# Optimization experiments

Hardware: AMD Instinct MI355X
Metric: run time of the kernel (lower is better)

The kernel has to match this reference:

```python
import jax, jax.numpy as jnp
import numpy as np

B, S, D = 2, 2048, 1024
H = 16
HD = D // H


def setup_inputs() -> dict:
    key = jax.random.key(0)
    ks = jax.random.split(key, 6)
    x = jax.random.normal(ks[0], (B, S, D), dtype=jnp.float32)
    scale = 1.0 / np.sqrt(D)
    Wq = jax.random.normal(ks[1], (D, D), dtype=jnp.float32) * scale
    Wk = jax.random.normal(ks[2], (D, D), dtype=jnp.float32) * scale
    Wv = jax.random.normal(ks[3], (D, D), dtype=jnp.float32) * scale
    Wo = jax.random.normal(ks[4], (D, D), dtype=jnp.float32) * scale
    bo = jax.random.normal(ks[5], (D,), dtype=jnp.float32) * 0.01
    return {"x": x, "Wq": Wq, "Wk": Wk, "Wv": Wv, "Wo": Wo, "bo": bo}


def reference(x, Wq, Wk, Wv, Wo, bo):
    b, t, _ = x.shape
    # QKV projections (no bias), split into heads: [b, h, t, hd]
    q = (x @ Wq).reshape(b, t, H, HD).transpose(0, 2, 1, 3)
    k = (x @ Wk).reshape(b, t, H, HD).transpose(0, 2, 1, 3)
    v = (x @ Wv).reshape(b, t, H, HD).transpose(0, 2, 1, 3)
    # scores [b, h, t, t]; causal mask (upper triangle -> -inf) applied before scaling
    scores = jnp.einsum("bhqd,bhkd->bhqk", q, k)
    causal = jnp.triu(jnp.ones((t, t), dtype=bool), k=1)
    scores = jnp.where(causal, -jnp.inf, scores)
    attn = jax.nn.softmax(scores / jnp.sqrt(jnp.asarray(HD, scores.dtype)), axis=-1)
    ctx = jnp.einsum("bhqk,bhkd->bhqd", attn, v)
    ctx = ctx.transpose(0, 2, 1, 3).reshape(b, t, H * HD)
    return ctx @ Wo + bo
```

## Files before the change

kernel.cpp:

```cpp
#include <hip/hip_runtime.h>

#define B_ 2
#define S_ 2048
#define D_ 1024
#define H_ 16
#define HD_ 64
#define M_ (B_*S_)

typedef __attribute__((ext_vector_type(8))) short bf16x8;
typedef __attribute__((ext_vector_type(4))) short s16x4;
typedef __attribute__((ext_vector_type(4))) float f32x4;
typedef __attribute__((ext_vector_type(4))) unsigned int u32x4;

static __device__ __forceinline__ unsigned short f2bf(float f) {
  unsigned int u = __builtin_bit_cast(unsigned int, f);
  u += 0x7FFFu + ((u >> 16) & 1u);
  return (unsigned short)(u >> 16);
}

static __device__ __forceinline__ unsigned int cvt_pk_bf16(float a, float b) {
  unsigned int r;
  asm("v_cvt_pk_bf16_f32 %0, %1, %2" : "=v"(r) : "v"(a), "v"(b));
  return r;
}

static __device__ __forceinline__ void gload_lds16(const void* g, void* l) {
  __builtin_amdgcn_global_load_lds(
      (const __attribute__((address_space(1))) unsigned int*)g,
      (__attribute__((address_space(3))) unsigned int*)l, 16, 0, 0);
}

__global__ __launch_bounds__(256) void xcvt_kernel(const float* __restrict__ x,
                                                   unsigned short* __restrict__ xb) {
  size_t i = ((size_t)blockIdx.x * 256 + threadIdx.x) * 8;
  float4 a = ((const float4*)(x + i))[0];
  float4 b = ((const float4*)(x + i))[1];
  bf16x8 w;
  w[0]=(short)f2bf(a.x); w[1]=(short)f2bf(a.y); w[2]=(short)f2bf(a.z); w[3]=(short)f2bf(a.w);
  w[4]=(short)f2bf(b.x); w[5]=(short)f2bf(b.y); w[6]=(short)f2bf(b.z); w[7]=(short)f2bf(b.w);
  *(bf16x8*)(xb + i) = w;
}

__global__ void wtrans_kernel(const float* __restrict__ Wq, const float* __restrict__ Wk,
                              const float* __restrict__ Wv, const float* __restrict__ Wo,
                              unsigned short* __restrict__ wt) {
  __shared__ float tile[32][33];
  const float* W = blockIdx.z==0 ? Wq : blockIdx.z==1 ? Wk : blockIdx.z==2 ? Wv : Wo;
  unsigned short* out = wt + (size_t)blockIdx.z * D_ * D_;
  int n0 = blockIdx.x*32, k0 = blockIdx.y*32;
  int tx = threadIdx.x, ty = threadIdx.y;
  #pragma unroll
  for (int i=0;i<4;i++) tile[ty+i*8][tx] = W[(size_t)(k0+ty+i*8)*D_ + n0+tx];
  __syncthreads();
  #pragma unroll
  for (int i=0;i<4;i++) out[(size_t)(n0+ty+i*8)*D_ + (k0+tx)] = f2bf(tile[tx][ty+i*8]);
}

#define GEMM_K_LOOP(Abase, Bbase)                                                     \
  for (int ks = 0; ks < 16; ++ks) {                                                   \
    const int k0 = ks * 64;                                                           \
    __syncthreads();                                                                  \
    _Pragma("unroll")                                                                 \
    for (int p = 0; p < 4; ++p) {                                                     \
      int c = p*256 + t;                                                              \
      int row = c >> 3, sl = (c & 7) ^ (row & 7);                                     \
      gload_lds16(Abase + (size_t)row*D_ + k0 + sl*8, &As[(p*256 + wid*64)*8]);       \
    }                                                                                 \
    _Pragma("unroll")                                                                 \
    for (int p = 0; p < 4; ++p) {                                                     \
      int c = p*256 + t;                                                              \
      int row = c >> 3, sl = (c & 7) ^ (row & 7);                                     \
      gload_lds16(Bbase + (size_t)row*D_ + k0 + sl*8, &Bs[(p*256 + wid*64)*8]);       \
    }                                                                                 \
    __syncthreads();                                                                  \
    _Pragma("unroll")                                                                 \
    for (int kk = 0; kk < 2; ++kk) {                                                  \
      bf16x8 af[4], bfr[4];                                                           \
      _Pragma("unroll")                                                               \
      for (int m = 0; m < 4; ++m) {                                                   \
        int row = wr + m*16 + l15;                                                    \
        af[m] = *(const bf16x8*)((const char*)As + row*128 + (((kk*4+lg)^(row&7))<<4)); \
      }                                                                               \
      _Pragma("unroll")                                                               \
      for (int n = 0; n < 4; ++n) {                                                   \
        int row = wc + n*16 + l15;                                                    \
        bfr[n] = *(const bf16x8*)((const char*)Bs + row*128 + (((kk*4+lg)^(row&7))<<4)); \
      }                                                                               \
      _Pragma("unroll")                                                               \
      for (int m = 0; m < 4; ++m)                                                     \
        _Pragma("unroll")                                                             \
        for (int n = 0; n < 4; ++n)                                                   \
          acc[m][n] = __builtin_amdgcn_mfma_f32_16x16x32_bf16(af[m], bfr[n], acc[m][n], 0,0,0); \
    }                                                                                 \
  }

__global__ __launch_bounds__(256,3) void gemm_qkv_kernel(
    const unsigned short* __restrict__ xb, const unsigned short* __restrict__ wt,
    unsigned short* __restrict__ Qo, unsigned short* __restrict__ Ko,
    unsigned short* __restrict__ Vto) {
  __shared__ __align__(16) unsigned short As[128*64];
  __shared__ __align__(16) unsigned short Bs[128*64];
  const int z = blockIdx.z;
  const int m0 = blockIdx.y*128, n0 = blockIdx.x*128;
  const int t = threadIdx.x, lane = t & 63, wid = t >> 6;
  const int wr = (wid>>1)*64, wc = (wid&1)*64;
  const int l15 = lane & 15, lg = lane >> 4;
  const unsigned short* Ab = xb + (size_t)m0 * D_;
  const unsigned short* Bb = wt + (size_t)z * D_ * D_ + (size_t)n0 * D_;

  f32x4 acc[4][4];
  #pragma unroll
  for (int m=0;m<4;m++)
    #pragma unroll
    for (int n=0;n<4;n++) acc[m][n] = f32x4{0.f,0.f,0.f,0.f};

  GEMM_K_LOOP(Ab, Bb)

  const float qscale = 0.18033688011112042f;
  #pragma unroll
  for (int m=0;m<4;m++) {
    #pragma unroll
    for (int n=0;n<4;n++) {
      #pragma unroll
      for (int r=0;r<4;r++) {
        int gm = m0 + wr + m*16 + lg*4 + r;
        int gn = n0 + wc + n*16 + l15;
        int b = gm >> 11, s = gm & (S_-1);
        int h = gn >> 6,  d = gn & 63;
        float av = acc[m][n][r];
        if (z==0) av *= qscale;
        unsigned short val = f2bf(av);
        if (z==0)      Qo[(((size_t)(b*H_+h))*S_ + s)*HD_ + d] = val;
        else if (z==1) Ko[(((size_t)(b*H_+h))*S_ + s)*HD_ + d] = val;
        else           Vto[(((size_t)(b*H_+h))*HD_ + d)*S_ + s] = val;
      }
    }
  }
}

__global__ __launch_bounds__(256,4) void attn_kernel(
    const unsigned short* __restrict__ Q, const unsigned short* __restrict__ K,
    const unsigned short* __restrict__ Vt, unsigned short* __restrict__ ctx) {
  __shared__ __align__(16) unsigned short KT[2][64*64];
  __shared__ __align__(16) unsigned short VT[2][64*64];
  const int t = threadIdx.x, lane = t & 63, wid = t >> 6;
  const int bh = blockIdx.x & 31;
  const int qt = 31 - (int)(blockIdx.x >> 5);
  const int b = bh >> 4, h = bh & 15;
  const int q0 = qt * 64, qw0 = q0 + wid * 16;
  const int nchunk = qt + 1;
  const unsigned short* Qp = Q  + (size_t)bh * S_ * HD_;
  const unsigned short* Kp = K  + (size_t)bh * S_ * HD_;
  const unsigned short* Vp = Vt + (size_t)bh * HD_ * S_;
  const int l15 = lane & 15, lg = lane >> 4;
  const int rsub = lane >> 3, slot = lane & 7;
  const int sslot = slot ^ rsub;

  bf16x8 qf0 = *(const bf16x8*)(Qp + (size_t)(qw0 + l15)*HD_ + lg*8);
  bf16x8 qf1 = *(const bf16x8*)(Qp + (size_t)(qw0 + l15)*HD_ + 32 + lg*8);

  f32x4 o[4];
  #pragma unroll
  for (int dt=0;dt<4;dt++) o[dt] = f32x4{0.f,0.f,0.f,0.f};
  float lsum = 0.f;

  auto stage = [&](int ch, int buf) {
    const int kk0 = ch * 64;
    #pragma unroll
    for (int j=0;j<2;j++) {
      int row = 16*wid + 8*j + rsub;
      gload_lds16(Kp + (size_t)(kk0 + row)*HD_ + sslot*8, &KT[buf][(16*wid + 8*j)*64]);
      gload_lds16(Vp + (size_t)row*S_ + kk0 + sslot*8,    &VT[buf][(16*wid + 8*j)*64]);
    }
  };

  stage(0, 0);
  __syncthreads();

  for (int ch=0; ch<nchunk; ++ch) {
    const int cur = ch & 1;
    const int kk0 = ch * 64;
    if (ch + 1 < nchunk) stage(ch+1, cur^1);

    const char* Kt = (const char*)&KT[cur][0];
    const char* Vv = (const char*)&VT[cur][0];

    f32x4 st[4];
    __builtin_amdgcn_s_setprio(1);
    #pragma unroll
    for (int kt=0; kt<4; ++kt) {
      int row = kt*16 + l15;
      int sw = (row & 7) << 4;
      bf16x8 kf0 = *(const bf16x8*)(Kt + row*128 + ((lg*16)      ^ sw));
      bf16x8 kf1 = *(const bf16x8*)(Kt + row*128 + ((64 + lg*16) ^ sw));
      f32x4 z = f32x4{0.f,0.f,0.f,0.f};
      z = __builtin_amdgcn_mfma_f32_16x16x32_bf16(kf0, qf0, z, 0,0,0);
      z = __builtin_amdgcn_mfma_f32_16x16x32_bf16(kf1, qf1, z, 0,0,0);
      st[kt] = z;
    }
    __builtin_amdgcn_s_setprio(0);

    if (ch == nchunk-1) {
      const int q = qw0 + l15;
      #pragma unroll
      for (int kt=0;kt<4;kt++)
        #pragma unroll
        for (int r=0;r<4;r++)
          if (kk0 + kt*16 + lg*4 + r > q) st[kt][r] = -INFINITY;
    }

    s16x4 pa[4];
    #pragma unroll
    for (int kt=0;kt<4;kt++) {
      #pragma unroll
      for (int r=0;r<4;r++) {
        float p = exp2f(st[kt][r]);
        st[kt][r] = p;
        lsum += p;
      }
      unsigned int plo = cvt_pk_bf16(st[kt][0], st[kt][1]);
      unsigned int phi = cvt_pk_bf16(st[kt][2], st[kt][3]);
      uint2 u; u.x = plo; u.y = phi;
      pa[kt] = __builtin_bit_cast(s16x4, u);
    }

    __builtin_amdgcn_s_setprio(1);
    #pragma unroll
    for (int dt=0;dt<4;dt++) {
      int row = dt*16 + l15;
      int sw = (row & 7) << 4;
      const char* vrow = Vv + row*128;
      #pragma unroll
      for (int kt=0;kt<4;kt++) {
        s16x4 vb = *(const s16x4*)(vrow + ((kt*32 + lg*8) ^ sw));
        o[dt] = __builtin_amdgcn_mfma_f32_16x16x16bf16_1k(pa[kt], vb, o[dt], 0,0,0);
      }
    }
    __builtin_amdgcn_s_setprio(0);

    __syncthreads();
  }

  lsum += __shfl_xor(lsum, 16);
  lsum += __shfl_xor(lsum, 32);
  float li = 1.f / lsum;
  float lr[4];
  #pragma unroll
  for (int r=0;r<4;r++) lr[r] = __shfl(li, lg*4 + r);
  #pragma unroll
  for (int dt=0;dt<4;dt++)
    #pragma unroll
    for (int r=0;r<4;r++) {
      size_t row = (size_t)(b*S_ + qw0 + lg*4 + r);
      ctx[row*D_ + h*HD_ + dt*16 + l15] = f2bf(o[dt][r] * lr[r]);
    }
}

__global__ __launch_bounds__(256,3) void gemm_out_kernel(
    const unsigned short* __restrict__ ctx, const unsigned short* __restrict__ WtO,
    const float* __restrict__ bo, float* __restrict__ out) {
  __shared__ __align__(16) unsigned short As[128*64];
  __shared__ __align__(16) unsigned short Bs[128*64];
  const int m0 = blockIdx.y*128, n0 = blockIdx.x*128;
  const int t = threadIdx.x, lane = t & 63, wid = t >> 6;
  const int wr = (wid>>1)*64, wc = (wid&1)*64;
  const int l15 = lane & 15, lg = lane >> 4;
  const unsigned short* Ab = ctx + (size_t)m0 * D_;
  const unsigned short* Bb = WtO + (size_t)n0 * D_;

  f32x4 acc[4][4];
  #pragma unroll
  for (int m=0;m<4;m++)
    #pragma unroll
    for (int n=0;n<4;n++) acc[m][n] = f32x4{0.f,0.f,0.f,0.f};

  GEMM_K_LOOP(Ab, Bb)

  #pragma unroll
  for (int n=0;n<4;n++) {
    float bias = bo[n0 + wc + n*16 + l15];
    #pragma unroll
    for (int m=0;m<4;m++)
      #pragma unroll
      for (int r=0;r<4;r++) {
        int gm = m0 + wr + m*16 + lg*4 + r;
        int gn = n0 + wc + n*16 + l15;
        out[(size_t)gm*D_ + gn] = acc[m][n][r] + bias;
      }
  }
}

extern "C" void kernel_launch(void* const* d_in, const int* in_sizes, int n_in,
                              void* d_out, int out_size, void* d_ws, size_t ws_size,
                              hipStream_t stream) {
  (void)in_sizes; (void)n_in; (void)out_size; (void)ws_size;
  const float* x  = (const float*)d_in[0];
  const float* Wq = (const float*)d_in[1];
  const float* Wk = (const float*)d_in[2];
  const float* Wv = (const float*)d_in[3];
  const float* Wo = (const float*)d_in[4];
  const float* bo = (const float*)d_in[5];
  float* out = (float*)d_out;

  unsigned short* wt  = (unsigned short*)d_ws;
  unsigned short* Qb  = wt  + (size_t)4*D_*D_;
  unsigned short* Kb  = Qb  + (size_t)M_*D_;
  unsigned short* Vtb = Kb  + (size_t)M_*D_;
  unsigned short* ctb = Vtb + (size_t)M_*D_;
  unsigned short* xbb = ctb + (size_t)M_*D_;

  xcvt_kernel<<<dim3(M_*D_/(256*8)), 256, 0, stream>>>(x, xbb);
  wtrans_kernel<<<dim3(32,32,4), dim3(32,8), 0, stream>>>(Wq, Wk, Wv, Wo, wt);
  gemm_qkv_kernel<<<dim3(8,32,3), 256, 0, stream>>>(xbb, wt, Qb, Kb, Vtb);
  attn_kernel<<<dim3(1024), 256, 0, stream>>>(Qb, Kb, Vtb, ctb);
  gemm_out_kernel<<<dim3(8,32), 256, 0, stream>>>(ctb, wt + (size_t)3*D_*D_, bo, out);
}
```

Measured before the change: 113.5 us.

## Pair causal query tiles per block to balance work and share K/V loads

Each attention block now handles two query tiles, pr and 31-pr, so every block performs the same total of 33 key chunks, and the grid is halved to 512 blocks. The K/V tiles staged in LDS are reused by both query tiles for the chunks they share, which cuts global/LDS traffic for those chunks. The cost is more registers per thread (two sets of accumulators and Q fragments), which may lower occupancy under the 256x4 launch bound, and fewer blocks to spread across the CUs.

```diff
diff --git a/kernel.cpp b/kernel.cpp
--- a/kernel.cpp
+++ b/kernel.cpp
@@ -1,4 +1,5 @@
 #include <hip/hip_runtime.h>
+#include <type_traits>
 
 #define B_ 2
 #define S_ 2048
@@ -145,10 +146,11 @@
   __shared__ __align__(16) unsigned short VT[2][64*64];
   const int t = threadIdx.x, lane = t & 63, wid = t >> 6;
   const int bh = blockIdx.x & 31;
-  const int qt = 31 - (int)(blockIdx.x >> 5);
+  const int pr = (int)(blockIdx.x >> 5);
   const int b = bh >> 4, h = bh & 15;
-  const int q0 = qt * 64, qw0 = q0 + wid * 16;
-  const int nchunk = qt + 1;
+  const int qA0 = pr*64 + wid*16;
+  const int qB0 = (31-pr)*64 + wid*16;
+  const int nA = pr + 1, nB = 32 - pr;
   const unsigned short* Qp = Q  + (size_t)bh * S_ * HD_;
   const unsigned short* Kp = K  + (size_t)bh * S_ * HD_;
   const unsigned short* Vp = Vt + (size_t)bh * HD_ * S_;
@@ -156,13 +158,15 @@
   const int rsub = lane >> 3, slot = lane & 7;
   const int sslot = slot ^ rsub;
 
-  bf16x8 qf0 = *(const bf16x8*)(Qp + (size_t)(qw0 + l15)*HD_ + lg*8);
-  bf16x8 qf1 = *(const bf16x8*)(Qp + (size_t)(qw0 + l15)*HD_ + 32 + lg*8);
-
-  f32x4 o[4];
-  #pragma unroll
-  for (int dt=0;dt<4;dt++) o[dt] = f32x4{0.f,0.f,0.f,0.f};
-  float lsum = 0.f;
+  bf16x8 qfA0 = *(const bf16x8*)(Qp + (size_t)(qA0 + l15)*HD_ + lg*8);
+  bf16x8 qfA1 = *(const bf16x8*)(Qp + (size_t)(qA0 + l15)*HD_ + 32 + lg*8);
+  bf16x8 qfB0 = *(const bf16x8*)(Qp + (size_t)(qB0 + l15)*HD_ + lg*8);
+  bf16x8 qfB1 = *(const bf16x8*)(Qp + (size_t)(qB0 + l15)*HD_ + 32 + lg*8);
+
+  f32x4 oA[4], oB[4];
+  #pragma unroll
+  for (int dt=0;dt<4;dt++) { oA[dt]=f32x4{0.f,0.f,0.f,0.f}; oB[dt]=f32x4{0.f,0.f,0.f,0.f}; }
+  float lsA = 0.f, lsB = 0.f;
 
   auto stage = [&](int ch, int buf) {
     const int kk0 = ch * 64;
@@ -174,18 +178,13 @@
     }
   };
 
-  stage(0, 0);
-  __syncthreads();
-
-  for (int ch=0; ch<nchunk; ++ch) {
-    const int cur = ch & 1;
+  auto chunk_body = [&](int ch, int cur, auto doA_c) {
+    constexpr bool DOA = decltype(doA_c)::value;
     const int kk0 = ch * 64;
-    if (ch + 1 < nchunk) stage(ch+1, cur^1);
-
     const char* Kt = (const char*)&KT[cur][0];
     const char* Vv = (const char*)&VT[cur][0];
 
-    f32x4 st[4];
+    f32x4 stA[4], stB[4];
     __builtin_amdgcn_s_setprio(1);
     #pragma unroll
     for (int kt=0; kt<4; ++kt) {
@@ -193,35 +192,52 @@
       int sw = (row & 7) << 4;
       bf16x8 kf0 = *(const bf16x8*)(Kt + row*128 + ((lg*16)      ^ sw));
       bf16x8 kf1 = *(const bf16x8*)(Kt + row*128 + ((64 + lg*16) ^ sw));
-      f32x4 z = f32x4{0.f,0.f,0.f,0.f};
-      z = __builtin_amdgcn_mfma_f32_16x16x32_bf16(kf0, qf0, z, 0,0,0);
-      z = __builtin_amdgcn_mfma_f32_16x16x32_bf16(kf1, qf1, z, 0,0,0);
-      st[kt] = z;
+      f32x4 zB = f32x4{0.f,0.f,0.f,0.f};
+      zB = __builtin_amdgcn_mfma_f32_16x16x32_bf16(kf0, qfB0, zB, 0,0,0);
+      zB = __builtin_amdgcn_mfma_f32_16x16x32_bf16(kf1, qfB1, zB, 0,0,0);
+      stB[kt] = zB;
+      if (DOA) {
+        f32x4 zA = f32x4{0.f,0.f,0.f,0.f};
+        zA = __builtin_amdgcn_mfma_f32_16x16x32_bf16(kf0, qfA0, zA, 0,0,0);
+        zA = __builtin_amdgcn_mfma_f32_16x16x32_bf16(kf1, qfA1, zA, 0,0,0);
+        stA[kt] = zA;
+      }
     }
     __builtin_amdgcn_s_setprio(0);
 
-    if (ch == nchunk-1) {
-      const int q = qw0 + l15;
+    if (ch == nB-1) {
+      const int q = qB0 + l15;
       #pragma unroll
       for (int kt=0;kt<4;kt++)
         #pragma unroll
         for (int r=0;r<4;r++)
-          if (kk0 + kt*16 + lg*4 + r > q) st[kt][r] = -INFINITY;
-    }
-
-    s16x4 pa[4];
+          if (kk0 + kt*16 + lg*4 + r > q) stB[kt][r] = -INFINITY;
+    }
+    if (DOA && ch == nA-1) {
+      const int q = qA0 + l15;
+      #pragma unroll
+      for (int kt=0;kt<4;kt++)
+        #pragma unroll
+        for (int r=0;r<4;r++)
+          if (kk0 + kt*16 + lg*4 + r > q) stA[kt][r] = -INFINITY;
+    }
+
+    s16x4 paA[4], paB[4];
     #pragma unroll
     for (int kt=0;kt<4;kt++) {
       #pragma unroll
       for (int r=0;r<4;r++) {
-        float p = exp2f(st[kt][r]);
-        st[kt][r] = p;
-        lsum += p;
-      }
-      unsigned int plo = cvt_pk_bf16(st[kt][0], st[kt][1]);
-      unsigned int phi = cvt_pk_bf16(st[kt][2], st[kt][3]);
-      uint2 u; u.x = plo; u.y = phi;
-      pa[kt] = __builtin_bit_cast(s16x4, u);
+        float p = exp2f(stB[kt][r]); stB[kt][r] = p; lsB += p;
+        if (DOA) { float pa = exp2f(stA[kt][r]); stA[kt][r] = pa; lsA += pa; }
+      }
+      uint2 uB; uB.x = cvt_pk_bf16(stB[kt][0], stB[kt][1]);
+      uB.y = cvt_pk_bf16(stB[kt][2], stB[kt][3]);
+      paB[kt] = __builtin_bit_cast(s16x4, uB);
+      if (DOA) {
+        uint2 uA; uA.x = cvt_pk_bf16(stA[kt][0], stA[kt][1]);
+        uA.y = cvt_pk_bf16(stA[kt][2], stA[kt][3]);
+        paA[kt] = __builtin_bit_cast(s16x4, uA);
+      }
     }
 
     __builtin_amdgcn_s_setprio(1);
@@ -233,27 +249,39 @@
       #pragma unroll
       for (int kt=0;kt<4;kt++) {
         s16x4 vb = *(const s16x4*)(vrow + ((kt*32 + lg*8) ^ sw));
-        o[dt] = __builtin_amdgcn_mfma_f32_16x16x16bf16_1k(pa[kt], vb, o[dt], 0,0,0);
+        oB[dt] = __builtin_amdgcn_mfma_f32_16x16x16bf16_1k(paB[kt], vb, oB[dt], 0,0,0);
+        if (DOA) oA[dt] = __builtin_amdgcn_mfma_f32_16x16x16bf16_1k(paA[kt], vb, oA[dt], 0,0,0);
       }
     }
     __builtin_amdgcn_s_setprio(0);
-
+  };
+
+  stage(0, 0);
+  __syncthreads();
+
+  for (int ch=0; ch<nB; ++ch) {
+    const int cur = ch & 1;
+    if (ch + 1 < nB) stage(ch+1, cur^1);
+    if (ch < nA) chunk_body(ch, cur, std::true_type{});
+    else         chunk_body(ch, cur, std::false_type{});
     __syncthreads();
   }
 
-  lsum += __shfl_xor(lsum, 16);
-  lsum += __shfl_xor(lsum, 32);
-  float li = 1.f / lsum;
-  float lr[4];
-  #pragma unroll
-  for (int r=0;r<4;r++) lr[r] = __shfl(li, lg*4 + r);
-  #pragma unroll
-  for (int dt=0;dt<4;dt++)
-    #pragma unroll
-    for (int r=0;r<4;r++) {
-      size_t row = (size_t)(b*S_ + qw0 + lg*4 + r);
-      ctx[row*D_ + h*HD_ + dt*16 + l15] = f2bf(o[dt][r] * lr[r]);
-    }
+  lsA += __shfl_xor(lsA, 16); lsA += __shfl_xor(lsA, 32);
+  lsB += __shfl_xor(lsB, 16); lsB += __shfl_xor(lsB, 32);
+  float liA = 1.f / lsA, liB = 1.f / lsB;
+  #pragma unroll
+  for (int r=0;r<4;r++) {
+    float lrA = __shfl(liA, lg*4 + r);
+    float lrB = __shfl(liB, lg*4 + r);
+    size_t rowA = (size_t)(b*S_ + qA0 + lg*4 + r);
+    size_t rowB = (size_t)(b*S_ + qB0 + lg*4 + r);
+    #pragma unroll
+    for (int dt=0;dt<4;dt++) {
+      ctx[rowA*D_ + h*HD_ + dt*16 + l15] = f2bf(oA[dt][r] * lrA);
+      ctx[rowB*D_ + h*HD_ + dt*16 + l15] = f2bf(oB[dt][r] * lrB);
+    }
+  }
 }
 
 __global__ __launch_bounds__(256,3) void gemm_out_kernel(
@@ -312,6 +340,6 @@
   xcvt_kernel<<<dim3(M_*D_/(256*8)), 256, 0, stream>>>(x, xbb);
   wtrans_kernel<<<dim3(32,32,4), dim3(32,8), 0, stream>>>(Wq, Wk, Wv, Wo, wt);
   gemm_qkv_kernel<<<dim3(8,32,3), 256, 0, stream>>>(xbb, wt, Qb, Kb, Vtb);
-  attn_kernel<<<dim3(1024), 256, 0, stream>>>(Qb, Kb, Vtb, ctb);
+  attn_kernel<<<dim3(512), 256, 0, stream>>>(Qb, Kb, Vtb, ctb);
   gemm_out_kernel<<<dim3(8,32), 256, 0, stream>>>(ctb, wt + (size_t)3*D_*D_, bo, out);
 }
```

New measurement: 133.8 us. 17.9% more time.

## Load K and V fragments directly from global memory in attention kernel

Applied to the files above, without the earlier changes.

Removes the double-buffered LDS staging of K and V tiles and the per-chunk block barrier; each wave now loads its MFMA operand fragments for K and V straight from global memory into registers. This eliminates shared-memory traffic and __syncthreads, freeing LDS for occupancy. In exchange, all four waves redundantly fetch the same K/V data from global/L2 with no prefetch overlap, and the V reads are narrower 8-byte strided accesses.

```diff
diff --git a/kernel.cpp b/kernel.cpp
--- a/kernel.cpp
+++ b/kernel.cpp
@@ -141,20 +141,16 @@
 __global__ __launch_bounds__(256,4) void attn_kernel(
     const unsigned short* __restrict__ Q, const unsigned short* __restrict__ K,
     const unsigned short* __restrict__ Vt, unsigned short* __restrict__ ctx) {
-  __shared__ __align__(16) unsigned short KT[2][64*64];
-  __shared__ __align__(16) unsigned short VT[2][64*64];
   const int t = threadIdx.x, lane = t & 63, wid = t >> 6;
   const int bh = blockIdx.x & 31;
   const int qt = 31 - (int)(blockIdx.x >> 5);
   const int b = bh >> 4, h = bh & 15;
-  const int q0 = qt * 64, qw0 = q0 + wid * 16;
+  const int qw0 = qt*64 + wid*16;
   const int nchunk = qt + 1;
   const unsigned short* Qp = Q  + (size_t)bh * S_ * HD_;
   const unsigned short* Kp = K  + (size_t)bh * S_ * HD_;
   const unsigned short* Vp = Vt + (size_t)bh * HD_ * S_;
   const int l15 = lane & 15, lg = lane >> 4;
-  const int rsub = lane >> 3, slot = lane & 7;
-  const int sslot = slot ^ rsub;
 
   bf16x8 qf0 = *(const bf16x8*)(Qp + (size_t)(qw0 + l15)*HD_ + lg*8);
   bf16x8 qf1 = *(const bf16x8*)(Qp + (size_t)(qw0 + l15)*HD_ + 32 + lg*8);
@@ -164,41 +160,36 @@
   for (int dt=0;dt<4;dt++) o[dt] = f32x4{0.f,0.f,0.f,0.f};
   float lsum = 0.f;
 
-  auto stage = [&](int ch, int buf) {
+  for (int ch=0; ch<nchunk; ++ch) {
     const int kk0 = ch * 64;
-    #pragma unroll
-    for (int j=0;j<2;j++) {
-      int row = 16*wid + 8*j + rsub;
-      gload_lds16(Kp + (size_t)(kk0 + row)*HD_ + sslot*8, &KT[buf][(16*wid + 8*j)*64]);
-      gload_lds16(Vp + (size_t)row*S_ + kk0 + sslot*8,    &VT[buf][(16*wid + 8*j)*64]);
-    }
-  };
-
-  stage(0, 0);
-  __syncthreads();
-
-  for (int ch=0; ch<nchunk; ++ch) {
-    const int cur = ch & 1;
-    const int kk0 = ch * 64;
-    if (ch + 1 < nchunk) stage(ch+1, cur^1);
-
-    const char* Kt = (const char*)&KT[cur][0];
-    const char* Vv = (const char*)&VT[cur][0];
+    const unsigned short* Kc = Kp + (size_t)kk0 * HD_;
+
+    bf16x8 kf0[4], kf1[4];
+    #pragma unroll
+    for (int kt=0;kt<4;kt++) {
+      kf0[kt] = *(const bf16x8*)(Kc + (size_t)(kt*16 + l15)*HD_ + lg*8);
+      kf1[kt] = *(const bf16x8*)(Kc + (size_t)(kt*16 + l15)*HD_ + 32 + lg*8);
+    }
 
     f32x4 st[4];
     __builtin_amdgcn_s_setprio(1);
     #pragma unroll
-    for (int kt=0; kt<4; ++kt) {
-      int row = kt*16 + l15;
-      int sw = (row & 7) << 4;
-      bf16x8 kf0 = *(const bf16x8*)(Kt + row*128 + ((lg*16)      ^ sw));
-      bf16x8 kf1 = *(const bf16x8*)(Kt + row*128 + ((64 + lg*16) ^ sw));
+    for (int kt=0;kt<4;kt++) {
       f32x4 z = f32x4{0.f,0.f,0.f,0.f};
-      z = __builtin_amdgcn_mfma_f32_16x16x32_bf16(kf0, qf0, z, 0,0,0);
-      z = __builtin_amdgcn_mfma_f32_16x16x32_bf16(kf1, qf1, z, 0,0,0);
+      z = __builtin_amdgcn_mfma_f32_16x16x32_bf16(kf0[kt], qf0, z, 0,0,0);
+      z = __builtin_amdgcn_mfma_f32_16x16x32_bf16(kf1[kt], qf1, z, 0,0,0);
       st[kt] = z;
     }
     __builtin_amdgcn_s_setprio(0);
+
+    s16x4 vb[4][4];
+    #pragma unroll
+    for (int dt=0;dt<4;dt++) {
+      const unsigned short* vrow = Vp + (size_t)(dt*16 + l15)*S_ + kk0;
+      #pragma unroll
+      for (int kt=0;kt<4;kt++)
+        vb[dt][kt] = *(const s16x4*)(vrow + kt*16 + lg*4);
+    }
 
     if (ch == nchunk-1) {
       const int q = qw0 + l15;
@@ -218,27 +209,19 @@
         st[kt][r] = p;
         lsum += p;
       }
-      unsigned int plo = cvt_pk_bf16(st[kt][0], st[kt][1]);
-      unsigned int phi = cvt_pk_bf16(st[kt][2], st[kt][3]);
-      uint2 u; u.x = plo; u.y = phi;
+      uint2 u;
+      u.x = cvt_pk_bf16(st[kt][0], st[kt][1]);
+      u.y = cvt_pk_bf16(st[kt][2], st[kt][3]);
       pa[kt] = __builtin_bit_cast(s16x4, u);
     }
 
     __builtin_amdgcn_s_setprio(1);
     #pragma unroll
-    for (int dt=0;dt<4;dt++) {
-      int row = dt*16 + l15;
-      int sw = (row & 7) << 4;
-      const char* vrow = Vv + row*128;
-      #pragma unroll
-      for (int kt=0;kt<4;kt++) {
-        s16x4 vb = *(const s16x4*)(vrow + ((kt*32 + lg*8) ^ sw));
-        o[dt] = __builtin_amdgcn_mfma_f32_16x16x16bf16_1k(pa[kt], vb, o[dt], 0,0,0);
-      }
-    }
+    for (int dt=0;dt<4;dt++)
+      #pragma unroll
+      for (int kt=0;kt<4;kt++)
+        o[dt] = __builtin_amdgcn_mfma_f32_16x16x16bf16_1k(pa[kt], vb[dt][kt], o[dt], 0,0,0);
     __builtin_amdgcn_s_setprio(0);
-
-    __syncthreads();
   }
 
   lsum += __shfl_xor(lsum, 16);
```

New measurement: 280.3 us. 2.47x slower.
